# Kernel tuning notes

Hardware: AMD Instinct MI355X
Metric: run time of the kernel (lower is better)

The kernel has to match this reference:

```python
import jax, jax.numpy as jnp
import numpy as np

B = 64            # number of graphs
N = 2048          # nodes per graph (equal segments; torch.stack in the original requires this)
D = 256           # hidden_dim
G = 4             # num_groups
SUBS = 3          # subclasses per group -> num_classes = 12
C = G * SUBS


def _layer_norm(x, g, b, eps=1e-5):
    mu = jnp.mean(x, axis=-1, keepdims=True)
    var = jnp.var(x, axis=-1, keepdims=True)
    return (x - mu) * jax.lax.rsqrt(var + eps) * g + b


def setup_inputs() -> dict:
    key = jax.random.key(0)
    ks = jax.random.split(key, 20)
    T = B * N
    inp = {
        "node_features": jax.random.normal(ks[0], (T, D), dtype=jnp.float32),
        "batch": jnp.repeat(jnp.arange(B, dtype=jnp.int64), N),  # sorted, equal-size segments
        # group queries (nn.Parameter randn)
        "group_queries": jax.random.normal(ks[1], (G, D), dtype=jnp.float32),
        # per-group projector MLP: D -> 2D -> SUBS*D (stacked over groups)
        "proj_w1": jax.random.normal(ks[2], (G, D, 2 * D), dtype=jnp.float32) * (1.0 / np.sqrt(D)),
        "proj_b1": jnp.zeros((G, 2 * D), dtype=jnp.float32),
        "proj_w2": jax.random.normal(ks[3], (G, 2 * D, SUBS * D), dtype=jnp.float32) * (1.0 / np.sqrt(2 * D)),
        "proj_b2": jnp.zeros((G, SUBS * D), dtype=jnp.float32),
        # output_proj_12: LN -> Linear(D, D//2) -> ReLU -> Linear(D//2, 1)
        "ln12_g": jnp.ones((D,), dtype=jnp.float32),
        "ln12_b": jnp.zeros((D,), dtype=jnp.float32),
        "w12a": jax.random.normal(ks[4], (D, D // 2), dtype=jnp.float32) * (1.0 / np.sqrt(D)),
        "b12a": jnp.zeros((D // 2,), dtype=jnp.float32),
        "w12b": jax.random.normal(ks[5], (D // 2, 1), dtype=jnp.float32) * (1.0 / np.sqrt(D // 2)),
        "b12b": jnp.zeros((1,), dtype=jnp.float32),
        # output_proj_4
        "ln4_g": jnp.ones((D,), dtype=jnp.float32),
        "ln4_b": jnp.zeros((D,), dtype=jnp.float32),
        "w4a": jax.random.normal(ks[6], (D, D // 2), dtype=jnp.float32) * (1.0 / np.sqrt(D)),
        "b4a": jnp.zeros((D // 2,), dtype=jnp.float32),
        "w4b": jax.random.normal(ks[7], (D // 2, 1), dtype=jnp.float32) * (1.0 / np.sqrt(D // 2)),
        "b4b": jnp.zeros((1,), dtype=jnp.float32),
    }
    return inp


def reference(node_features, batch, group_queries, proj_w1, proj_b1, proj_w2, proj_b2,
              ln12_g, ln12_b, w12a, b12a, w12b, b12b,
              ln4_g, ln4_b, w4a, b4a, w4b, b4b):
    # --- derive class queries from group queries (per-group MLP) ---
    h = jax.nn.relu(jnp.einsum('gd,gdh->gh', group_queries, proj_w1) + proj_b1)   # [G, 2D]
    flat = jnp.einsum('gh,ghk->gk', h, proj_w2) + proj_b2                         # [G, SUBS*D]
    # group g maps to global class indices [3g, 3g+1, 3g+2] -> simple reshape gives ordered queries
    class_queries = flat.reshape(C, D)                                            # [12, D]

    scale = jnp.asarray(D ** 0.5, node_features.dtype)
    # equal-size sorted segments: reshape total nodes into [B, N, D] per-graph blocks
    nodes = node_features.reshape(B, N, D)

    # --- 12-class attention pooling ---
    scores12 = jnp.einsum('cd,bnd->bcn', class_queries, nodes) / scale            # [B, 12, N]
    attn12 = jax.nn.softmax(scores12, axis=-1)
    pooled12 = jnp.einsum('bcn,bnd->bcd', attn12, nodes)                          # [B, 12, D]
    x12 = _layer_norm(pooled12, ln12_g, ln12_b)
    logits_12 = (jax.nn.relu(x12 @ w12a + b12a) @ w12b + b12b)[..., 0]            # [B, 12]

    # --- 4-group attention pooling ---
    scores4 = jnp.einsum('gd,bnd->bgn', group_queries, nodes) / scale             # [B, 4, N]
    attn4 = jax.nn.softmax(scores4, axis=-1)
    pooled4 = jnp.einsum('bgn,bnd->bgd', attn4, nodes)                            # [B, 4, D]
    x4 = _layer_norm(pooled4, ln4_g, ln4_b)
    logits_4 = (jax.nn.relu(x4 @ w4a + b4a) @ w4b + b4b)[..., 0]                  # [B, 4]

    return (logits_12, logits_4, attn12)
```

## Files before the change

kernel.cpp:

```cpp
#include <hip/hip_runtime.h>
#include <math.h>

#define BG   64
#define NN   2048
#define DD   256
#define CQ   16
#define NCH  8

static constexpr size_t WS_Q16 = 0;
static constexpr size_t WS_H   = 4096;
static constexpr size_t WS_S   = 6144;
static constexpr size_t WS_ML  = WS_S + (size_t)BG * CQ * NN;
static constexpr size_t WS_PL  = WS_ML + (size_t)BG * NCH * 32;
static constexpr size_t WS_FML = WS_PL + (size_t)BG * NCH * CQ * DD;
static constexpr size_t WS_FIL = WS_FML + 1024;

__global__ __launch_bounds__(256) void kA1(const float* __restrict__ gq,
                                           const float* __restrict__ w1,
                                           const float* __restrict__ b1,
                                           float* __restrict__ ws) {
    int blk = blockIdx.x;
    int g   = blk >> 4;
    int jb  = (blk & 15) * 32;
    int t   = threadIdx.x;
    __shared__ float qlds[256];
    qlds[t] = gq[g * 256 + t];
    if ((blk & 15) == 0) ws[WS_Q16 + (12 + g) * 256 + t] = gq[g * 256 + t];
    __syncthreads();
    int jl = t & 31, dp = t >> 5;
    float acc = 0.f;
    const float* wp = w1 + ((size_t)g * 256) * 512 + jb + jl;
    #pragma unroll 8
    for (int i = 0; i < 32; ++i) {
        int d = dp * 32 + i;
        acc += qlds[d] * wp[(size_t)d * 512];
    }
    __shared__ float red[8][33];
    red[dp][jl] = acc;
    __syncthreads();
    if (dp == 0) {
        float s = 0.f;
        #pragma unroll
        for (int p = 0; p < 8; ++p) s += red[p][jl];
        s += b1[g * 512 + jb + jl];
        ws[WS_H + g * 512 + jb + jl] = fmaxf(s, 0.f);
    }
}

__global__ __launch_bounds__(256) void kA2(const float* __restrict__ w2,
                                           const float* __restrict__ b2,
                                           float* __restrict__ ws) {
    int blk = blockIdx.x;
    int g   = blk / 48;
    int kb  = (blk % 48) * 16;
    int t   = threadIdx.x;
    __shared__ float hlds[512];
    hlds[t]       = ws[WS_H + g * 512 + t];
    hlds[t + 256] = ws[WS_H + g * 512 + t + 256];
    __syncthreads();
    int kl = t & 15, dp = t >> 4;
    float acc = 0.f;
    const float* wp = w2 + ((size_t)g * 512) * 768 + kb + kl;
    #pragma unroll 8
    for (int i = 0; i < 32; ++i) {
        int jj = dp * 32 + i;
        acc += hlds[jj] * wp[(size_t)jj * 768];
    }
    __shared__ float red[16][17];
    red[dp][kl] = acc;
    __syncthreads();
    if (dp == 0) {
        float s = 0.f;
        #pragma unroll
        for (int p = 0; p < 16; ++p) s += red[p][kl];
        ws[WS_Q16 + g * 768 + kb + kl] = s + b2[g * 768 + kb + kl];
    }
}

__global__ __launch_bounds__(256) void kF(const float* __restrict__ x,
                                          float* __restrict__ ws) {
    __shared__ float4 qlds[CQ * 64];
    __shared__ float  wlds[CQ * 256];
    __shared__ float  mbuf[CQ], lbuf[CQ];

    int t   = threadIdx.x;
    int blk = blockIdx.x;
    int b   = blk >> 3, ch = blk & 7;
    int gn0 = b * NN + ch * 256;

    const float4* qg = (const float4*)(ws + WS_Q16);
    #pragma unroll
    for (int i = 0; i < 4; ++i) qlds[t + i * 256] = qg[t + i * 256];
    __syncthreads();

    const float4* xa = (const float4*)x + (size_t)(gn0 + t) * 64;
    float sc[CQ];
    #pragma unroll
    for (int c = 0; c < CQ; ++c) sc[c] = 0.f;

    float4 buf[8];
    #pragma unroll
    for (int i = 0; i < 8; ++i) buf[i] = xa[i];
    for (int base = 0; base < 64; base += 8) {
        float4 cur[8];
        #pragma unroll
        for (int i = 0; i < 8; ++i) cur[i] = buf[i];
        if (base + 8 < 64) {
            #pragma unroll
            for (int i = 0; i < 8; ++i) buf[i] = xa[base + 8 + i];
        }
        #pragma unroll
        for (int i = 0; i < 8; ++i) {
            #pragma unroll
            for (int c = 0; c < CQ; ++c) {
                float4 q = qlds[c * 64 + base + i];
                sc[c] += q.x * cur[i].x + q.y * cur[i].y
                       + q.z * cur[i].z + q.w * cur[i].w;
            }
        }
    }
    #pragma unroll
    for (int c = 0; c < CQ; ++c) sc[c] *= 0.0625f;

    float* srow = ws + WS_S + ((size_t)b * CQ) * NN + ch * 256;
    #pragma unroll
    for (int c = 0; c < CQ; ++c) srow[(size_t)c * NN + t] = sc[c];

    #pragma unroll
    for (int c = 0; c < CQ; ++c) wlds[c * 256 + t] = sc[c];
    __syncthreads();
    {
        int c = t >> 4, slot = t & 15;
        float mv = -1e30f;
        #pragma unroll
        for (int k = 0; k < 16; ++k) mv = fmaxf(mv, wlds[c * 256 + slot + k * 16]);
        #pragma unroll
        for (int off = 1; off < 16; off <<= 1) mv = fmaxf(mv, __shfl_xor(mv, off, 64));
        if (slot == 0) mbuf[c] = mv;
    }
    __syncthreads();
    #pragma unroll
    for (int c = 0; c < CQ; ++c) wlds[c * 256 + t] = __expf(sc[c] - mbuf[c]);
    __syncthreads();
    {
        int c = t >> 4, slot = t & 15;
        float lv = 0.f;
        #pragma unroll
        for (int k = 0; k < 16; ++k) lv += wlds[c * 256 + slot + k * 16];
        #pragma unroll
        for (int off = 1; off < 16; off <<= 1) lv += __shfl_xor(lv, off, 64);
        if (slot == 0) lbuf[c] = lv;
    }
    __syncthreads();
    if (t < CQ) {
        ws[WS_ML + (size_t)blk * 32 + t]      = mbuf[t];
        ws[WS_ML + (size_t)blk * 32 + 16 + t] = lbuf[t];
    }

    int wave = t >> 6, lane = t & 63;
    float4 acc[CQ];
    #pragma unroll
    for (int c = 0; c < CQ; ++c) acc[c] = make_float4(0.f, 0.f, 0.f, 0.f);

    const float4* xq = (const float4*)x + (size_t)(gn0 + wave * 64) * 64 + lane;
    for (int nq = 0; nq < 16; ++nq) {
        float4 x0 = xq[(size_t)(nq * 4 + 0) * 64];
        float4 x1 = xq[(size_t)(nq * 4 + 1) * 64];
        float4 x2 = xq[(size_t)(nq * 4 + 2) * 64];
        float4 x3 = xq[(size_t)(nq * 4 + 3) * 64];
        #pragma unroll
        for (int c = 0; c < CQ; ++c) {
            float4 ev = *(const float4*)&wlds[c * 256 + wave * 64 + nq * 4];
            acc[c].x += ev.x * x0.x + ev.y * x1.x + ev.z * x2.x + ev.w * x3.x;
            acc[c].y += ev.x * x0.y + ev.y * x1.y + ev.z * x2.y + ev.w * x3.y;
            acc[c].z += ev.x * x0.z + ev.y * x1.z + ev.z * x2.z + ev.w * x3.z;
            acc[c].w += ev.x * x0.w + ev.y * x1.w + ev.z * x2.w + ev.w * x3.w;
        }
    }

    float* sdata = (float*)qlds;
    __syncthreads();
    for (int w = 0; w < 4; ++w) {
        if (wave == w) {
            #pragma unroll
            for (int c = 0; c < CQ; ++c) {
                float* dst = &sdata[c * 256 + lane * 4];
                if (w == 0) {
                    dst[0] = acc[c].x; dst[1] = acc[c].y;
                    dst[2] = acc[c].z; dst[3] = acc[c].w;
                } else {
                    dst[0] += acc[c].x; dst[1] += acc[c].y;
                    dst[2] += acc[c].z; dst[3] += acc[c].w;
                }
            }
        }
        __syncthreads();
    }
    float* po = ws + WS_PL + (size_t)blk * (CQ * 256);
    #pragma unroll
    for (int i = 0; i < CQ; ++i) po[t + i * 256] = sdata[t + i * 256];
}

__global__ __launch_bounds__(256) void kE(float* __restrict__ ws,
        const float* __restrict__ lnG12, const float* __restrict__ lnB12,
        const float* __restrict__ wA12,  const float* __restrict__ bA12,
        const float* __restrict__ wB12,  const float* __restrict__ bB12,
        const float* __restrict__ lnG4,  const float* __restrict__ lnB4,
        const float* __restrict__ wA4,   const float* __restrict__ bA4,
        const float* __restrict__ wB4,   const float* __restrict__ bB4,
        float* __restrict__ out) {
    int bc = blockIdx.x;
    int b = bc >> 4, c = bc & 15;
    int t = threadIdx.x, wave = t >> 6, lane = t & 63;

    __shared__ float scl[NCH];
    __shared__ float sinvl;
    if (t == 0) {
        float mi[NCH], li[NCH];
        float m = -1e30f;
        for (int i = 0; i < NCH; ++i) {
            mi[i] = ws[WS_ML + (size_t)(b * NCH + i) * 32 + c];
            li[i] = ws[WS_ML + (size_t)(b * NCH + i) * 32 + 16 + c];
            m = fmaxf(m, mi[i]);
        }
        float l = 0.f;
        for (int i = 0; i < NCH; ++i) {
            float s = __expf(mi[i] - m);
            scl[i] = s;
            l += s * li[i];
        }
        float il = 1.f / l;
        sinvl = il;
        ws[WS_FML + bc] = m;
        ws[WS_FIL + bc] = il;
    }
    __syncthreads();

    float v = 0.f;
    for (int i = 0; i < NCH; ++i)
        v += scl[i] * ws[WS_PL + ((size_t)(b * NCH + i) * CQ + c) * 256 + t];
    v *= sinvl;

    __shared__ float wr1[4], wr2[4];
    float s = v;
    #pragma unroll
    for (int off = 32; off; off >>= 1) s += __shfl_xor(s, off, 64);
    if (lane == 0) wr1[wave] = s;
    __syncthreads();
    float mu = (wr1[0] + wr1[1] + wr1[2] + wr1[3]) * (1.f / 256.f);
    float dv = v - mu;
    s = dv * dv;
    #pragma unroll
    for (int off = 32; off; off >>= 1) s += __shfl_xor(s, off, 64);
    if (lane == 0) wr2[wave] = s;
    __syncthreads();
    float var = (wr2[0] + wr2[1] + wr2[2] + wr2[3]) * (1.f / 256.f);

    bool is12 = (c < 12);
    const float* lg = is12 ? lnG12 : lnG4;
    const float* lb = is12 ? lnB12 : lnB4;
    const float* wA = is12 ? wA12  : wA4;
    const float* bA = is12 ? bA12  : bA4;
    const float* wB = is12 ? wB12  : wB4;
    const float* bB = is12 ? bB12  : bB4;

    __shared__ float ylds[256];
    __shared__ float hred[256];
    __shared__ float hlds[128];
    float y = dv * rsqrtf(var + 1e-5f) * lg[t] + lb[t];
    ylds[t] = y;
    __syncthreads();
    {
        int j = t & 127, half = t >> 7;
        float hh = 0.f;
        const float* wc = wA + (size_t)half * 128 * 128 + j;
        #pragma unroll 4
        for (int d = 0; d < 128; ++d) hh += ylds[half * 128 + d] * wc[(size_t)d * 128];
        hred[t] = hh;
    }
    __syncthreads();
    if (t < 128) hlds[t] = fmaxf(hred[t] + hred[t + 128] + bA[t], 0.f);
    __syncthreads();
    if (t < 64) {
        float pp = hlds[t] * wB[t] + hlds[t + 64] * wB[t + 64];
        #pragma unroll
        for (int off = 32; off; off >>= 1) pp += __shfl_xor(pp, off, 64);
        if (t == 0) {
            float logit = pp + bB[0];
            if (is12) out[b * 12 + c] = logit;
            else      out[768 + b * 4 + (c - 12)] = logit;
        }
    }
}

__global__ __launch_bounds__(256) void kAttn(const float* __restrict__ ws,
                                             float* __restrict__ out_attn) {
    int blk = blockIdx.x;
    int b = blk / 12, c = blk % 12;
    int t = threadIdx.x;
    float m  = ws[WS_FML + b * 16 + c];
    float il = ws[WS_FIL + b * 16 + c];
    const float4* sr = (const float4*)(ws + WS_S + ((size_t)b * CQ + c) * NN);
    float4* ar = (float4*)out_attn + (size_t)(b * 12 + c) * (NN / 4);
    #pragma unroll
    for (int k = 0; k < 2; ++k) {
        float4 v = sr[t + k * 256];
        float4 e;
        e.x = __expf(v.x - m) * il;
        e.y = __expf(v.y - m) * il;
        e.z = __expf(v.z - m) * il;
        e.w = __expf(v.w - m) * il;
        ar[t + k * 256] = e;
    }
}

extern "C" void kernel_launch(void* const* d_in, const int* in_sizes, int n_in,
                              void* d_out, int out_size, void* d_ws, size_t ws_size,
                              hipStream_t stream) {
    const float* x     = (const float*)d_in[0];
    const float* gq    = (const float*)d_in[2];
    const float* w1    = (const float*)d_in[3];
    const float* b1    = (const float*)d_in[4];
    const float* w2    = (const float*)d_in[5];
    const float* b2    = (const float*)d_in[6];
    const float* ln12g = (const float*)d_in[7];
    const float* ln12b = (const float*)d_in[8];
    const float* w12a  = (const float*)d_in[9];
    const float* b12a  = (const float*)d_in[10];
    const float* w12b  = (const float*)d_in[11];
    const float* b12b  = (const float*)d_in[12];
    const float* ln4g  = (const float*)d_in[13];
    const float* ln4b  = (const float*)d_in[14];
    const float* w4a   = (const float*)d_in[15];
    const float* b4a   = (const float*)d_in[16];
    const float* w4b   = (const float*)d_in[17];
    const float* b4b   = (const float*)d_in[18];

    float* out = (float*)d_out;
    float* ws  = (float*)d_ws;

    kA1  <<<64,       256, 0, stream>>>(gq, w1, b1, ws);
    kA2  <<<192,      256, 0, stream>>>(w2, b2, ws);
    kF   <<<BG * NCH, 256, 0, stream>>>(x, ws);
    kE   <<<1024,     256, 0, stream>>>(ws,
            ln12g, ln12b, w12a, b12a, w12b, b12b,
            ln4g,  ln4b,  w4a,  b4a,  w4b,  b4b, out);
    kAttn<<<768,      256, 0, stream>>>(ws, out + 1024);
}
```

Measured before the change: 290.6 us.

## Split node chunks finer in kF, fuse attention output into kE

The main fused kernel now handles 128-node chunks instead of 256, which doubles the block count to 1024. The score dot product is split across two thread halves over D, and the pooling accumulation is split across query groups and node groups, which cuts per-thread accumulator registers and adds an occupancy hint of 4. Only the 12 class score rows are stored to workspace, and the separate attention-normalisation kernel is folded into kE, which removes one launch and a workspace round trip. The costs are more partial results for kE to merge (16 chunks instead of 8) and an extra LDS pass for the score reduction.

```diff
diff --git a/kernel.cpp b/kernel.cpp
--- a/kernel.cpp
+++ b/kernel.cpp
@@ -5,15 +5,14 @@
 #define NN   2048
 #define DD   256
 #define CQ   16
-#define NCH  8
+#define CS   128
+#define NCH  16
 
 static constexpr size_t WS_Q16 = 0;
 static constexpr size_t WS_H   = 4096;
 static constexpr size_t WS_S   = 6144;
-static constexpr size_t WS_ML  = WS_S + (size_t)BG * CQ * NN;
+static constexpr size_t WS_ML  = WS_S + (size_t)BG * 12 * NN;
 static constexpr size_t WS_PL  = WS_ML + (size_t)BG * NCH * 32;
-static constexpr size_t WS_FML = WS_PL + (size_t)BG * NCH * CQ * DD;
-static constexpr size_t WS_FIL = WS_FML + 1024;
 
 __global__ __launch_bounds__(256) void kA1(const float* __restrict__ gq,
                                            const float* __restrict__ w1,
@@ -77,23 +76,24 @@
     }
 }
 
-__global__ __launch_bounds__(256) void kF(const float* __restrict__ x,
-                                          float* __restrict__ ws) {
+__global__ __launch_bounds__(256, 4) void kF(const float* __restrict__ x,
+                                             float* __restrict__ ws) {
     __shared__ float4 qlds[CQ * 64];
-    __shared__ float  wlds[CQ * 256];
+    __shared__ float  wlds[CQ * CS];
     __shared__ float  mbuf[CQ], lbuf[CQ];
 
     int t   = threadIdx.x;
     int blk = blockIdx.x;
-    int b   = blk >> 3, ch = blk & 7;
-    int gn0 = b * NN + ch * 256;
+    int b   = blk >> 4, ch = blk & 15;
+    int gn0 = b * NN + ch * CS;
 
     const float4* qg = (const float4*)(ws + WS_Q16);
     #pragma unroll
     for (int i = 0; i < 4; ++i) qlds[t + i * 256] = qg[t + i * 256];
     __syncthreads();
 
-    const float4* xa = (const float4*)x + (size_t)(gn0 + t) * 64;
+    int node = t & 127, half = t >> 7;
+    const float4* xa = (const float4*)x + (size_t)(gn0 + node) * 64 + half * 32;
     float sc[CQ];
     #pragma unroll
     for (int c = 0; c < CQ; ++c) sc[c] = 0.f;
@@ -101,11 +101,11 @@
     float4 buf[8];
     #pragma unroll
     for (int i = 0; i < 8; ++i) buf[i] = xa[i];
-    for (int base = 0; base < 64; base += 8) {
+    for (int base = 0; base < 32; base += 8) {
         float4 cur[8];
         #pragma unroll
         for (int i = 0; i < 8; ++i) cur[i] = buf[i];
-        if (base + 8 < 64) {
+        if (base + 8 < 32) {
             #pragma unroll
             for (int i = 0; i < 8; ++i) buf[i] = xa[base + 8 + i];
         }
@@ -113,40 +113,55 @@
         for (int i = 0; i < 8; ++i) {
             #pragma unroll
             for (int c = 0; c < CQ; ++c) {
-                float4 q = qlds[c * 64 + base + i];
+                float4 q = qlds[c * 64 + half * 32 + base + i];
                 sc[c] += q.x * cur[i].x + q.y * cur[i].y
                        + q.z * cur[i].z + q.w * cur[i].w;
             }
         }
     }
-    #pragma unroll
-    for (int c = 0; c < CQ; ++c) sc[c] *= 0.0625f;
-
-    float* srow = ws + WS_S + ((size_t)b * CQ) * NN + ch * 256;
-    #pragma unroll
-    for (int c = 0; c < CQ; ++c) srow[(size_t)c * NN + t] = sc[c];
-
-    #pragma unroll
-    for (int c = 0; c < CQ; ++c) wlds[c * 256 + t] = sc[c];
-    __syncthreads();
+
+    if (half == 1) {
+        #pragma unroll
+        for (int c = 0; c < CQ; ++c) wlds[c * CS + node] = sc[c];
+    }
+    __syncthreads();
+    if (half == 0) {
+        #pragma unroll
+        for (int c = 0; c < CQ; ++c)
+            wlds[c * CS + node] = (sc[c] + wlds[c * CS + node]) * 0.0625f;
+    }
+    __syncthreads();
+
+    {
+        float* srow = ws + WS_S + (size_t)b * 12 * NN + ch * CS;
+        #pragma unroll
+        for (int k = 0; k < 6; ++k) {
+            int idx = k * 256 + t;
+            srow[(size_t)(idx >> 7) * NN + (idx & 127)] = wlds[idx];
+        }
+    }
+
     {
         int c = t >> 4, slot = t & 15;
         float mv = -1e30f;
         #pragma unroll
-        for (int k = 0; k < 16; ++k) mv = fmaxf(mv, wlds[c * 256 + slot + k * 16]);
+        for (int k = 0; k < 8; ++k) mv = fmaxf(mv, wlds[c * CS + slot + k * 16]);
         #pragma unroll
         for (int off = 1; off < 16; off <<= 1) mv = fmaxf(mv, __shfl_xor(mv, off, 64));
         if (slot == 0) mbuf[c] = mv;
     }
     __syncthreads();
     #pragma unroll
-    for (int c = 0; c < CQ; ++c) wlds[c * 256 + t] = __expf(sc[c] - mbuf[c]);
+    for (int k = 0; k < 8; ++k) {
+        int idx = k * 256 + t;
+        wlds[idx] = __expf(wlds[idx] - mbuf[idx >> 7]);
+    }
     __syncthreads();
     {
         int c = t >> 4, slot = t & 15;
         float lv = 0.f;
         #pragma unroll
-        for (int k = 0; k < 16; ++k) lv += wlds[c * 256 + slot + k * 16];
+        for (int k = 0; k < 8; ++k) lv += wlds[c * CS + slot + k * 16];
         #pragma unroll
         for (int off = 1; off < 16; off <<= 1) lv += __shfl_xor(lv, off, 64);
         if (slot == 0) lbuf[c] = lv;
@@ -158,47 +173,48 @@
     }
 
     int wave = t >> 6, lane = t & 63;
-    float4 acc[CQ];
-    #pragma unroll
-    for (int c = 0; c < CQ; ++c) acc[c] = make_float4(0.f, 0.f, 0.f, 0.f);
-
-    const float4* xq = (const float4*)x + (size_t)(gn0 + wave * 64) * 64 + lane;
+    int ng = wave & 1, cg = wave >> 1;
+    float4 acc[8];
+    #pragma unroll
+    for (int j = 0; j < 8; ++j) acc[j] = make_float4(0.f, 0.f, 0.f, 0.f);
+
+    const float4* xq = (const float4*)x + (size_t)(gn0 + ng * 64) * 64 + lane;
     for (int nq = 0; nq < 16; ++nq) {
         float4 x0 = xq[(size_t)(nq * 4 + 0) * 64];
         float4 x1 = xq[(size_t)(nq * 4 + 1) * 64];
         float4 x2 = xq[(size_t)(nq * 4 + 2) * 64];
         float4 x3 = xq[(size_t)(nq * 4 + 3) * 64];
         #pragma unroll
-        for (int c = 0; c < CQ; ++c) {
-            float4 ev = *(const float4*)&wlds[c * 256 + wave * 64 + nq * 4];
-            acc[c].x += ev.x * x0.x + ev.y * x1.x + ev.z * x2.x + ev.w * x3.x;
-            acc[c].y += ev.x * x0.y + ev.y * x1.y + ev.z * x2.y + ev.w * x3.y;
-            acc[c].z += ev.x * x0.z + ev.y * x1.z + ev.z * x2.z + ev.w * x3.z;
-            acc[c].w += ev.x * x0.w + ev.y * x1.w + ev.z * x2.w + ev.w * x3.w;
-        }
-    }
-
-    float* sdata = (float*)qlds;
-    __syncthreads();
-    for (int w = 0; w < 4; ++w) {
-        if (wave == w) {
-            #pragma unroll
-            for (int c = 0; c < CQ; ++c) {
-                float* dst = &sdata[c * 256 + lane * 4];
-                if (w == 0) {
-                    dst[0] = acc[c].x; dst[1] = acc[c].y;
-                    dst[2] = acc[c].z; dst[3] = acc[c].w;
-                } else {
-                    dst[0] += acc[c].x; dst[1] += acc[c].y;
-                    dst[2] += acc[c].z; dst[3] += acc[c].w;
-                }
-            }
-        }
-        __syncthreads();
-    }
+        for (int j = 0; j < 8; ++j) {
+            int c = cg * 8 + j;
+            float4 ev = *(const float4*)&wlds[c * CS + ng * 64 + nq * 4];
+            acc[j].x += ev.x * x0.x + ev.y * x1.x + ev.z * x2.x + ev.w * x3.x;
+            acc[j].y += ev.x * x0.y + ev.y * x1.y + ev.z * x2.y + ev.w * x3.y;
+            acc[j].z += ev.x * x0.z + ev.y * x1.z + ev.z * x2.z + ev.w * x3.z;
+            acc[j].w += ev.x * x0.w + ev.y * x1.w + ev.z * x2.w + ev.w * x3.w;
+        }
+    }
+
+    float4* sdata = qlds;
+    if (ng == 0) {
+        #pragma unroll
+        for (int j = 0; j < 8; ++j) sdata[(cg * 8 + j) * 64 + lane] = acc[j];
+    }
+    __syncthreads();
+    if (ng == 1) {
+        #pragma unroll
+        for (int j = 0; j < 8; ++j) {
+            float4* p = &sdata[(cg * 8 + j) * 64 + lane];
+            float4 v = *p;
+            v.x += acc[j].x; v.y += acc[j].y; v.z += acc[j].z; v.w += acc[j].w;
+            *p = v;
+        }
+    }
+    __syncthreads();
     float* po = ws + WS_PL + (size_t)blk * (CQ * 256);
-    #pragma unroll
-    for (int i = 0; i < CQ; ++i) po[t + i * 256] = sdata[t + i * 256];
+    const float* sf = (const float*)sdata;
+    #pragma unroll
+    for (int i = 0; i < CQ; ++i) po[t + i * 256] = sf[t + i * 256];
 }
 
 __global__ __launch_bounds__(256) void kE(float* __restrict__ ws,
@@ -214,25 +230,22 @@
     int t = threadIdx.x, wave = t >> 6, lane = t & 63;
 
     __shared__ float scl[NCH];
-    __shared__ float sinvl;
-    if (t == 0) {
-        float mi[NCH], li[NCH];
-        float m = -1e30f;
-        for (int i = 0; i < NCH; ++i) {
-            mi[i] = ws[WS_ML + (size_t)(b * NCH + i) * 32 + c];
-            li[i] = ws[WS_ML + (size_t)(b * NCH + i) * 32 + 16 + c];
-            m = fmaxf(m, mi[i]);
-        }
-        float l = 0.f;
-        for (int i = 0; i < NCH; ++i) {
-            float s = __expf(mi[i] - m);
-            scl[i] = s;
-            l += s * li[i];
-        }
-        float il = 1.f / l;
-        sinvl = il;
-        ws[WS_FML + bc] = m;
-        ws[WS_FIL + bc] = il;
+    __shared__ float sinvl, smv;
+    if (t < NCH) {
+        float mi = ws[WS_ML + (size_t)(b * NCH + t) * 32 + c];
+        float li = ws[WS_ML + (size_t)(b * NCH + t) * 32 + 16 + c];
+        float m = mi;
+        #pragma unroll
+        for (int off = 1; off < 16; off <<= 1) m = fmaxf(m, __shfl_xor(m, off, 64));
+        float e = __expf(mi - m);
+        float pl = e * li;
+        #pragma unroll
+        for (int off = 1; off < 16; off <<= 1) pl += __shfl_xor(pl, off, 64);
+        scl[t] = e;
+        if (t == 0) {
+            sinvl = 1.f / pl;
+            smv   = m;
+        }
     }
     __syncthreads();
 
@@ -240,6 +253,23 @@
     for (int i = 0; i < NCH; ++i)
         v += scl[i] * ws[WS_PL + ((size_t)(b * NCH + i) * CQ + c) * 256 + t];
     v *= sinvl;
+
+    if (c < 12) {
+        float m  = smv;
+        float il = sinvl;
+        const float4* sr = (const float4*)(ws + WS_S + ((size_t)b * 12 + c) * NN);
+        float4* ar = (float4*)(out + 1024) + ((size_t)b * 12 + c) * (NN / 4);
+        #pragma unroll
+        for (int k = 0; k < 2; ++k) {
+            float4 s4 = sr[t + k * 256];
+            float4 e4;
+            e4.x = __expf(s4.x - m) * il;
+            e4.y = __expf(s4.y - m) * il;
+            e4.z = __expf(s4.z - m) * il;
+            e4.w = __expf(s4.w - m) * il;
+            ar[t + k * 256] = e4;
+        }
+    }
 
     __shared__ float wr1[4], wr2[4];
     float s = v;
@@ -290,27 +320,6 @@
             if (is12) out[b * 12 + c] = logit;
             else      out[768 + b * 4 + (c - 12)] = logit;
         }
-    }
-}
-
-__global__ __launch_bounds__(256) void kAttn(const float* __restrict__ ws,
-                                             float* __restrict__ out_attn) {
-    int blk = blockIdx.x;
-    int b = blk / 12, c = blk % 12;
-    int t = threadIdx.x;
-    float m  = ws[WS_FML + b * 16 + c];
-    float il = ws[WS_FIL + b * 16 + c];
-    const float4* sr = (const float4*)(ws + WS_S + ((size_t)b * CQ + c) * NN);
-    float4* ar = (float4*)out_attn + (size_t)(b * 12 + c) * (NN / 4);
-    #pragma unroll
-    for (int k = 0; k < 2; ++k) {
-        float4 v = sr[t + k * 256];
-        float4 e;
-        e.x = __expf(v.x - m) * il;
-        e.y = __expf(v.y - m) * il;
-        e.z = __expf(v.z - m) * il;
-        e.w = __expf(v.w - m) * il;
-        ar[t + k * 256] = e;
     }
 }
 
@@ -339,11 +348,10 @@
     float* out = (float*)d_out;
     float* ws  = (float*)d_ws;
 
-    kA1  <<<64,       256, 0, stream>>>(gq, w1, b1, ws);
-    kA2  <<<192,      256, 0, stream>>>(w2, b2, ws);
-    kF   <<<BG * NCH, 256, 0, stream>>>(x, ws);
-    kE   <<<1024,     256, 0, stream>>>(ws,
+    kA1<<<64,       256, 0, stream>>>(gq, w1, b1, ws);
+    kA2<<<192,      256, 0, stream>>>(w2, b2, ws);
+    kF <<<BG * NCH, 256, 0, stream>>>(x, ws);
+    kE <<<1024,     256, 0, stream>>>(ws,
             ln12g, ln12b, w12a, b12a, w12b, b12b,
             ln4g,  ln4b,  w4a,  b4a,  w4b,  b4b, out);
-    kAttn<<<768,      256, 0, stream>>>(ws, out + 1024);
-}
+}
```

After: 280.4 us. 1.04x faster.
